# Optimization experiments

Hardware: AMD Instinct MI355X
Metric: run time of the kernel (lower is better)

The kernel has to match this reference:

```python
import jax, jax.numpy as jnp
import numpy as np

B, S, D, H = 4, 8192, 1024, 16
DH = D // H  # attention head size


def setup_inputs() -> dict:
    key = jax.random.key(0)
    ks = jax.random.split(key, 12)
    sc = 0.02
    return {
        "hidden_states": jax.random.normal(ks[0], (B, S, D), jnp.float32),
        "attention_mask": jnp.zeros((B, 1, S), jnp.float32),
        "Wq": jax.random.normal(ks[1], (D, D), jnp.float32) * sc,
        "bq": jnp.zeros((D,), jnp.float32),
        "Wqa": jax.random.normal(ks[2], (D, H), jnp.float32) * sc,
        "bqa": jnp.zeros((H,), jnp.float32),
        "Wk": jax.random.normal(ks[3], (D, D), jnp.float32) * sc,
        "bk": jnp.zeros((D,), jnp.float32),
        "Wka": jax.random.normal(ks[4], (D, H), jnp.float32) * sc,
        "bka": jnp.zeros((H,), jnp.float32),
        "Wt": jax.random.normal(ks[5], (D, D), jnp.float32) * sc,
        "bt": jnp.zeros((D,), jnp.float32),
    }


def reference(hidden_states, attention_mask, Wq, bq, Wqa, bqa, Wk, bk, Wka, bka, Wt, bt):
    b, s, _ = hidden_states.shape
    scale = 1.0 / np.sqrt(DH).astype(np.float32)

    mixed_q = hidden_states @ Wq + bq            # [B,S,D]
    mixed_k = hidden_states @ Wk + bk            # [B,S,D]

    # query attention pooling: scores [B,H,S]
    q_score = (mixed_q @ Wqa + bqa).transpose(0, 2, 1) * scale + attention_mask
    q_weight = jax.nn.softmax(q_score, axis=-1)  # [B,H,S]

    q_heads = mixed_q.reshape(b, s, H, DH)       # [B,S,H,DH]
    pooled_q = jnp.einsum("bhs,bshd->bhd", q_weight, q_heads)  # [B,H,DH]
    pooled_q = pooled_q.reshape(b, 1, D)         # global query vector per batch

    mixed_qk = mixed_k * pooled_q                # [B,S,D]

    qk_score = (mixed_qk @ Wka + bka).transpose(0, 2, 1) * scale + attention_mask
    qk_weight = jax.nn.softmax(qk_score, axis=-1)  # [B,H,S]

    k_heads = mixed_qk.reshape(b, s, H, DH)
    pooled_k = jnp.einsum("bhs,bshd->bhd", qk_weight, k_heads)  # [B,H,DH]

    weighted = (q_heads * pooled_k[:, None, :, :]).reshape(b, s, D)  # [B,S,D]
    return weighted @ Wt + bt + mixed_q
```

## Files before the change

### kernel.cpp

```cpp
#include <hip/hip_runtime.h>
#include <hip/hip_bf16.h>
#include <stdint.h>

typedef __hip_bfloat16 bf16;
typedef __attribute__((ext_vector_type(8))) short bf16x8v;
typedef __attribute__((ext_vector_type(4))) float f32x4v;

#define B_   4
#define S_   8192
#define D_   1024
#define H_   16
#define DH_  64
#define M_TOT (B_ * S_)

__device__ __forceinline__ float bf2f(bf16 x) { return __bfloat162float(x); }
__device__ __forceinline__ bf16  f2bf(float x) { return __float2bfloat16(x); }

__device__ __forceinline__ void storev(float* p, float v) { *p = v; }
__device__ __forceinline__ void storev(bf16* p, float v) { *p = f2bf(v); }

__device__ __forceinline__ void async_copy16(const void* g, void* l) {
  __builtin_amdgcn_global_load_lds(
      (const __attribute__((address_space(1))) unsigned int*)g,
      (__attribute__((address_space(3))) unsigned int*)l,
      16, 0, 0);
}

#define VMCNT(n) asm volatile("s_waitcnt vmcnt(" #n ")" ::: "memory")
__device__ __forceinline__ void barrier_() {
  asm volatile("" ::: "memory");
  __builtin_amdgcn_s_barrier();
  asm volatile("" ::: "memory");
}

__global__ __launch_bounds__(256) void prep_kernel(
    const float* __restrict__ hs, const float* __restrict__ Wq,
    const float* __restrict__ Wk, const float* __restrict__ Wqa,
    bf16* __restrict__ hs_bf, bf16* __restrict__ WqkT, bf16* __restrict__ WaqT)
{
  __shared__ float tset[32][33];
  const int blk = blockIdx.x, tid = threadIdx.x;
  if (blk < 2048) {
    const int n4 = M_TOT * D_ / 4;
    for (int i = blk * 256 + tid; i < n4; i += 2048 * 256) {
      const float4 v = ((const float4*)hs)[i];
      union { bf16 h[4]; uint64_t u; } pk;
      pk.h[0] = f2bf(v.x); pk.h[1] = f2bf(v.y);
      pk.h[2] = f2bf(v.z); pk.h[3] = f2bf(v.w);
      ((uint64_t*)hs_bf)[i] = pk.u;
    }
  } else if (blk < 4096) {
    const int t = blk - 2048;
    const int mat = t >> 10, tile = t & 1023;
    const int bx = tile & 31, by = tile >> 5;
    const float* W = mat ? Wk : Wq;
    bf16* o = WqkT + (size_t)mat * 1024 * 1024;
    const int tx = tid & 31, ty0 = tid >> 5;
#pragma unroll
    for (int r = 0; r < 4; ++r)
      tset[ty0 + 8 * r][tx] = W[(size_t)(by * 32 + ty0 + 8 * r) * D_ + bx * 32 + tx];
    __syncthreads();
#pragma unroll
    for (int r = 0; r < 4; ++r)
      o[(size_t)(bx * 32 + ty0 + 8 * r) * D_ + by * 32 + tx] = f2bf(tset[tx][ty0 + 8 * r]);
  } else {
    const int idx = (blk - 4096) * 256 + tid;
    const int d = idx & (D_ - 1), h = (idx >> 10) & 15;
    WaqT[idx] = f2bf(Wqa[d * H_ + h]);
  }
}

#define STAGE_A(nb, h, k0) do { \
  async_copy16(gA + (size_t)((h) * 64      ) * sA + (size_t)(k0) * 2, smem + (nb) + (h) * 16384 + ldsw); \
  async_copy16(gA + (size_t)((h) * 64 + 128) * sA + (size_t)(k0) * 2, smem + (nb) + (h) * 16384 + 8192 + ldsw); \
} while (0)

#define STAGE_B(nb, h, k0) do { \
  async_copy16(gB + (size_t)((h) * 32      ) * sB + (size_t)(k0) * 2, smem + (nb) + 32768 + (h) * 16384 + ldsw); \
  async_copy16(gB + (size_t)((h) * 32 + 128) * sB + (size_t)(k0) * 2, smem + (nb) + 32768 + (h) * 16384 + 8192 + ldsw); \
} while (0)

#define READ_A(mh) do { \
  _Pragma("unroll") for (int il = 0; il < 4; ++il) { \
    const uint8_t* p_ = Ab + (mh) * 16384 + (wr * 64 + il * 16 + l16) * 128; \
    a[il][0] = *(const bf16x8v*)(p_ + k0off); \
    a[il][1] = *(const bf16x8v*)(p_ + k1off); } \
} while (0)

#define READ_B(nh, BR) do { \
  _Pragma("unroll") for (int jl = 0; jl < 2; ++jl) { \
    const uint8_t* p_ = Bb + 32768 + (nh) * 16384 + (wc * 32 + jl * 16 + l16) * 128; \
    BR[jl][0] = *(const bf16x8v*)(p_ + k0off); \
    BR[jl][1] = *(const bf16x8v*)(p_ + k1off); } \
} while (0)

#define MFMA_Q(IOFF, JOFF, BR) do { \
  _Pragma("unroll") for (int il = 0; il < 4; ++il) \
  _Pragma("unroll") for (int jl = 0; jl < 2; ++jl) \
  _Pragma("unroll") for (int kk = 0; kk < 2; ++kk) \
    acc[(IOFF) + il][(JOFF) + jl] = __builtin_amdgcn_mfma_f32_16x16x32_bf16( \
        a[il][kk], BR[jl][kk], acc[(IOFF) + il][(JOFF) + jl], 0, 0, 0); \
} while (0)

template <typename OutT>
__global__ __launch_bounds__(512, 2) void gemm256_kernel(
    const bf16* __restrict__ A, int lda, const bf16* __restrict__ BT,
    const float* __restrict__ bias0, const float* __restrict__ bias1,
    const bf16* addC, int ldadd,
    OutT* __restrict__ C, int ldc, int M, int Ncols, int K, int perBatchB)
{
  extern __shared__ __align__(16) uint8_t smem[];

  const int ntile = Ncols >> 8;
  const int mtiles = M >> 8;
  const int xcd = blockIdx.x & 7;
  const int local = blockIdx.x >> 3;
  const int tn = local % ntile;
  const int tm = xcd * (mtiles >> 3) + local / ntile;
  const int m0 = tm << 8, n0 = tn << 8;
  const bf16* Bt = BT + (perBatchB ? (size_t)(m0 >> 13) * (size_t)Ncols * (size_t)K : 0);

  const int tid = threadIdx.x, w = tid >> 6, lane = tid & 63;
  const int quad = lane >> 4, l16 = lane & 15;
  const int wr = w >> 2, wc = w & 3;
  const int lr = lane >> 3, ls = lane & 7;

  const size_t sA = (size_t)lda * 2, sB = (size_t)K * 2;
  const int srcslot = (ls ^ lr) << 4;
  const uint8_t* gA = (const uint8_t*)A  + (size_t)(m0 + 8 * w + lr) * sA + srcslot;
  const uint8_t* gB = (const uint8_t*)Bt + (size_t)(n0 + 64 * wr + 8 * wc + lr) * sB + srcslot;
  const int ldsw = w << 10;

  const int e7 = l16 & 7;
  const int k0off = (quad ^ e7) << 4;
  const int k1off = ((quad + 4) ^ e7) << 4;

  f32x4v acc[8][4] = {};
  bf16x8v a[4][2], b0[2][2], b1[2][2];

  const int NT = K >> 6;

  STAGE_A(0, 0, 0);
  STAGE_B(0, 0, 0);
  STAGE_B(0, 1, 0);
  STAGE_A(0, 1, 0);
  VMCNT(4);
  barrier_();

  for (int t = 0; t < NT; ++t) {
    const int buf = (t & 1) << 16;
    const int nbuf = buf ^ 65536;
    const int kst = (t + 1 < NT ? t + 1 : t) << 6;
    const uint8_t* Ab = smem + buf;
    const uint8_t* Bb = smem + buf;

    READ_A(0);
    READ_B(0, b0);
    STAGE_A(nbuf, 0, kst);
    barrier_();
    __builtin_amdgcn_s_setprio(1);
    MFMA_Q(0, 0, b0);
    __builtin_amdgcn_s_setprio(0);
    VMCNT(4);
    barrier_();

    READ_B(1, b1);
    STAGE_B(nbuf, 0, kst);
    barrier_();
    __builtin_amdgcn_s_setprio(1);
    MFMA_Q(0, 2, b1);
    __builtin_amdgcn_s_setprio(0);
    VMCNT(4);
    barrier_();

    READ_A(1);
    STAGE_B(nbuf, 1, kst);
    barrier_();
    __builtin_amdgcn_s_setprio(1);
    MFMA_Q(4, 2, b1);
    __builtin_amdgcn_s_setprio(0);
    barrier_();

    STAGE_A(nbuf, 1, kst);
    barrier_();
    __builtin_amdgcn_s_setprio(1);
    MFMA_Q(4, 0, b0);
    __builtin_amdgcn_s_setprio(0);
    VMCNT(4);
    barrier_();
  }
  VMCNT(0);

#pragma unroll
  for (int ai = 0; ai < 8; ++ai) {
    const int row = m0 + wr * 128 + ai * 16 + quad * 4;
#pragma unroll
    for (int jb = 0; jb < 4; ++jb) {
      const int col = n0 + wc * 64 + jb * 16 + l16;
      const float bb = (col < 1024) ? (bias0 ? bias0[col] : 0.f)
                                    : (bias1 ? bias1[col - 1024] : 0.f);
      f32x4v v = acc[ai][jb];
#pragma unroll
      for (int r = 0; r < 4; ++r) {
        float o = v[r] + bb;
        if (addC) o += bf2f(addC[(size_t)(row + r) * ldadd + col]);
        storev(&C[(size_t)(row + r) * ldc + col], o);
      }
    }
  }
}

__global__ __launch_bounds__(256) void score_kernel(
    const bf16* __restrict__ X, int ldx, const bf16* __restrict__ WaT,
    const float* __restrict__ mask, float* __restrict__ scores,
    float scale, int perBatchW)
{
  const int tid = threadIdx.x, wave = tid >> 6, lane = tid & 63;
  const int quad = lane >> 4, l16 = lane & 15;
  const int row0 = blockIdx.x * 64 + wave * 16;
  const int b = row0 / S_;
  const bf16* W = WaT + (perBatchW ? (size_t)b * H_ * D_ : 0);
  const bf16* arow = X + (size_t)(row0 + l16) * ldx;
  const bf16* brow = W + (size_t)l16 * D_;
  f32x4v acc = {};
  for (int k0 = 0; k0 < D_; k0 += 32) {
    bf16x8v av = *(const bf16x8v*)(arow + k0 + quad * 8);
    bf16x8v bv = *(const bf16x8v*)(brow + k0 + quad * 8);
    acc = __builtin_amdgcn_mfma_f32_16x16x32_bf16(av, bv, acc, 0, 0, 0);
  }
  const int srel = (row0 % S_) + quad * 4;
  const float* mp = mask + (size_t)b * S_ + srel;
  float* orow = scores + ((size_t)b * H_ + l16) * S_ + srel;
#pragma unroll
  for (int r = 0; r < 4; r++) orow[r] = expf(acc[r] * scale + mp[r]);
}

__global__ __launch_bounds__(256) void pool_kernel(
    const float* __restrict__ esc, const bf16* __restrict__ X, int ldx,
    float* __restrict__ pooled, float* __restrict__ sumw)
{
  const int bh = blockIdx.x, chunk = blockIdx.y;
  const int b = bh >> 4, h = bh & 15;
  const int dh = threadIdx.x & 63, sr = threadIdx.x >> 6;
  const float* erow = esc + (size_t)bh * S_;
  float acc = 0.f, accw = 0.f;
  const int s0 = chunk * 256;
  for (int s = s0 + sr; s < s0 + 256; s += 4) {
    const float e = erow[s];
    acc += e * bf2f(X[((size_t)b * S_ + s) * ldx + h * DH_ + dh]);
    if (dh == 0) accw += e;
  }
  __shared__ float red[256];
  __shared__ float rw[4];
  red[threadIdx.x] = acc;
  if (dh == 0) rw[sr] = accw;
  __syncthreads();
  if (sr == 0)
    atomicAdd(&pooled[b * D_ + h * DH_ + dh],
              red[dh] + red[64 + dh] + red[128 + dh] + red[192 + dh]);
  if (threadIdx.x == 0)
    atomicAdd(&sumw[bh], rw[0] + rw[1] + rw[2] + rw[3]);
}

__global__ __launch_bounds__(256) void prep_wa_kernel(
    const float* __restrict__ Wa, const float* __restrict__ pq,
    const float* __restrict__ sw, bf16* __restrict__ out)
{
  const int idx = blockIdx.x * 256 + threadIdx.x;
  if (idx >= B_ * H_ * D_) return;
  const int d = idx & (D_ - 1);
  const int h = (idx >> 10) & 15;
  const int b = idx >> 14;
  const float inv = __frcp_rn(sw[b * H_ + (d >> 6)]);
  const float v = Wa[d * H_ + h] * pq[b * D_ + d] * inv;
  out[idx] = f2bf(v);
}

__global__ __launch_bounds__(1024) void transpose_scale_kernel(
    const float* __restrict__ W, const float* __restrict__ pq,
    const float* __restrict__ swq, const float* __restrict__ pk,
    const float* __restrict__ swk, bf16* __restrict__ out)
{
  __shared__ float t[32][33];
  const int tx = threadIdx.x, ty = threadIdx.y;
  const int bx = blockIdx.x, by = blockIdx.y, b = blockIdx.z;
  t[ty][tx] = W[(size_t)(by * 32 + ty) * D_ + bx * 32 + tx];
  __syncthreads();
  const int n = bx * 32 + ty, k = by * 32 + tx;
  const float invq = __frcp_rn(swq[b * H_ + (k >> 6)]);
  const float invk = __frcp_rn(swk[b * H_ + (k >> 6)]);
  const float s = (pq[b * D_ + k] * invq) * (pk[b * D_ + k] * invk);
  out[(size_t)b * D_ * D_ + (size_t)n * D_ + k] = f2bf(t[tx][ty] * s);
}

namespace {
struct LdsAttrInit {
  LdsAttrInit() {
    (void)hipFuncSetAttribute(reinterpret_cast<const void*>(&gemm256_kernel<bf16>),
                              hipFuncAttributeMaxDynamicSharedMemorySize, 131072);
    (void)hipFuncSetAttribute(reinterpret_cast<const void*>(&gemm256_kernel<float>),
                              hipFuncAttributeMaxDynamicSharedMemorySize, 131072);
  }
};
LdsAttrInit ldsAttrInit_;
}

extern "C" void kernel_launch(void* const* d_in, const int* in_sizes, int n_in,
                              void* d_out, int out_size, void* d_ws, size_t ws_size,
                              hipStream_t stream)
{
  const float* hs   = (const float*)d_in[0];
  const float* mask = (const float*)d_in[1];
  const float* Wq   = (const float*)d_in[2];
  const float* bq   = (const float*)d_in[3];
  const float* Wqa  = (const float*)d_in[4];
  const float* Wk   = (const float*)d_in[6];
  const float* bk   = (const float*)d_in[7];
  const float* Wka  = (const float*)d_in[8];
  const float* Wt   = (const float*)d_in[10];
  const float* bt   = (const float*)d_in[11];
  float* out = (float*)d_out;

  uint8_t* w = (uint8_t*)d_ws;
  bf16*  hs_bf     = (bf16*)(w + 0);
  bf16*  mixed_qk  = (bf16*)(w + 67108864);
  bf16*  WqkT      = (bf16*)(w + 201326592);
  bf16*  WtTs      = (bf16*)(w + 205520896);
  bf16*  WaqT      = (bf16*)(w + 213909504);
  bf16*  WakTs     = (bf16*)(w + 213942272);
  float* scores_q  = (float*)(w + 214073344);
  float* scores_qk = (float*)(w + 216170496);
  float* pq_raw    = (float*)(w + 218267648);
  float* pk_raw    = (float*)(w + 218284032);
  float* sumw_q    = (float*)(w + 218300416);
  float* sumw_k    = (float*)(w + 218300672);

  const bf16* mixed_q = mixed_qk;
  const bf16* mixed_k = mixed_qk + 1024;
  const int LDQK = 2048;

  const float scale = 0.125f;
  dim3 tblk(32, 32);

  hipMemsetAsync(pq_raw, 0, 2 * 16384 + 512, stream);

  prep_kernel<<<4160, 256, 0, stream>>>(hs, Wq, Wk, Wqa, hs_bf, WqkT, WaqT);

  gemm256_kernel<bf16><<<1024, 512, 131072, stream>>>(
      hs_bf, 1024, WqkT, bq, bk, nullptr, 0, mixed_qk, LDQK, M_TOT, 2048, D_, 0);

  score_kernel<<<512, 256, 0, stream>>>(mixed_q, LDQK, WaqT, mask, scores_q, scale, 0);
  pool_kernel<<<dim3(64, 32), 256, 0, stream>>>(scores_q, mixed_q, LDQK, pq_raw, sumw_q);

  prep_wa_kernel<<<256, 256, 0, stream>>>(Wka, pq_raw, sumw_q, WakTs);
  score_kernel<<<512, 256, 0, stream>>>(mixed_k, LDQK, WakTs, mask, scores_qk, scale, 1);
  pool_kernel<<<dim3(64, 32), 256, 0, stream>>>(scores_qk, mixed_k, LDQK, pk_raw, sumw_k);

  transpose_scale_kernel<<<dim3(32, 32, 4), tblk, 0, stream>>>(
      Wt, pq_raw, sumw_q, pk_raw, sumw_k, WtTs);

  gemm256_kernel<float><<<512, 512, 131072, stream>>>(
      mixed_q, LDQK, WtTs, bt, nullptr, mixed_q, LDQK, out, D_, M_TOT, D_, D_, 1);
}
```

Measured before the change: 608.5 us.

## Fuse attention score and pooling kernels to avoid re-reading activations

Merges the score computation and the weighted pooling into one kernel. Each block computes exp-scores for its 64 rows in LDS and immediately accumulates the weighted sum over the same rows, which are likely still cache-hot. This removes the intermediate score buffers and a second full pass over mixed_q/mixed_k. The cost is more atomicAdds, one per column per 64-row block instead of one per column per 256-row chunk, plus a block barrier.

```diff
diff --git a/kernel.cpp b/kernel.cpp
--- a/kernel.cpp
+++ b/kernel.cpp
@@ -15,6 +15,10 @@
 
 __device__ __forceinline__ float bf2f(bf16 x) { return __bfloat162float(x); }
 __device__ __forceinline__ bf16  f2bf(float x) { return __float2bfloat16(x); }
+__device__ __forceinline__ float u16tof(unsigned short u) {
+  const unsigned int x = ((unsigned int)u) << 16;
+  return __builtin_bit_cast(float, x);
+}
 
 __device__ __forceinline__ void storev(float* p, float v) { *p = v; }
 __device__ __forceinline__ void storev(bf16* p, float v) { *p = f2bf(v); }
@@ -210,17 +214,19 @@
   }
 }
 
-__global__ __launch_bounds__(256) void score_kernel(
+__global__ __launch_bounds__(256) void score_pool_kernel(
     const bf16* __restrict__ X, int ldx, const bf16* __restrict__ WaT,
-    const float* __restrict__ mask, float* __restrict__ scores,
-    float scale, int perBatchW)
-{
+    const float* __restrict__ mask, float* __restrict__ pooled,
+    float* __restrict__ sumw, float scale, int perBatchW)
+{
+  __shared__ float e_lds[16][65];
   const int tid = threadIdx.x, wave = tid >> 6, lane = tid & 63;
   const int quad = lane >> 4, l16 = lane & 15;
-  const int row0 = blockIdx.x * 64 + wave * 16;
+  const int row0 = blockIdx.x * 64;
   const int b = row0 / S_;
   const bf16* W = WaT + (perBatchW ? (size_t)b * H_ * D_ : 0);
-  const bf16* arow = X + (size_t)(row0 + l16) * ldx;
+
+  const bf16* arow = X + (size_t)(row0 + wave * 16 + l16) * ldx;
   const bf16* brow = W + (size_t)l16 * D_;
   f32x4v acc = {};
   for (int k0 = 0; k0 < D_; k0 += 32) {
@@ -228,38 +234,37 @@
     bf16x8v bv = *(const bf16x8v*)(brow + k0 + quad * 8);
     acc = __builtin_amdgcn_mfma_f32_16x16x32_bf16(av, bv, acc, 0, 0, 0);
   }
-  const int srel = (row0 % S_) + quad * 4;
-  const float* mp = mask + (size_t)b * S_ + srel;
-  float* orow = scores + ((size_t)b * H_ + l16) * S_ + srel;
-#pragma unroll
-  for (int r = 0; r < 4; r++) orow[r] = expf(acc[r] * scale + mp[r]);
-}
-
-__global__ __launch_bounds__(256) void pool_kernel(
-    const float* __restrict__ esc, const bf16* __restrict__ X, int ldx,
-    float* __restrict__ pooled, float* __restrict__ sumw)
-{
-  const int bh = blockIdx.x, chunk = blockIdx.y;
-  const int b = bh >> 4, h = bh & 15;
-  const int dh = threadIdx.x & 63, sr = threadIdx.x >> 6;
-  const float* erow = esc + (size_t)bh * S_;
-  float acc = 0.f, accw = 0.f;
-  const int s0 = chunk * 256;
-  for (int s = s0 + sr; s < s0 + 256; s += 4) {
-    const float e = erow[s];
-    acc += e * bf2f(X[((size_t)b * S_ + s) * ldx + h * DH_ + dh]);
-    if (dh == 0) accw += e;
-  }
-  __shared__ float red[256];
-  __shared__ float rw[4];
-  red[threadIdx.x] = acc;
-  if (dh == 0) rw[sr] = accw;
+  const int srel = wave * 16 + quad * 4;
+  const float* mp = mask + row0 + srel;
+#pragma unroll
+  for (int r = 0; r < 4; ++r)
+    e_lds[l16][srel + r] = expf(acc[r] * scale + mp[r]);
   __syncthreads();
-  if (sr == 0)
-    atomicAdd(&pooled[b * D_ + h * DH_ + dh],
-              red[dh] + red[64 + dh] + red[128 + dh] + red[192 + dh]);
-  if (threadIdx.x == 0)
-    atomicAdd(&sumw[bh], rw[0] + rw[1] + rw[2] + rw[3]);
+
+  const int c0 = tid * 4;
+  const int h = c0 >> 6;
+  float p0 = 0.f, p1 = 0.f, p2 = 0.f, p3 = 0.f;
+  const bf16* xb = X + (size_t)row0 * ldx + c0;
+#pragma unroll 4
+  for (int s = 0; s < 64; ++s) {
+    const float e = e_lds[h][s];
+    const ushort4 xv = *(const ushort4*)(xb + (size_t)s * ldx);
+    p0 += e * u16tof(xv.x);
+    p1 += e * u16tof(xv.y);
+    p2 += e * u16tof(xv.z);
+    p3 += e * u16tof(xv.w);
+  }
+  float* pd = pooled + (size_t)b * D_ + c0;
+  atomicAdd(pd + 0, p0);
+  atomicAdd(pd + 1, p1);
+  atomicAdd(pd + 2, p2);
+  atomicAdd(pd + 3, p3);
+  if (tid < 16) {
+    float sum = 0.f;
+#pragma unroll 8
+    for (int s = 0; s < 64; ++s) sum += e_lds[tid][s];
+    atomicAdd(&sumw[b * H_ + tid], sum);
+  }
 }
 
 __global__ __launch_bounds__(256) void prep_wa_kernel(
@@ -328,8 +333,6 @@
   bf16*  WtTs      = (bf16*)(w + 205520896);
   bf16*  WaqT      = (bf16*)(w + 213909504);
   bf16*  WakTs     = (bf16*)(w + 213942272);
-  float* scores_q  = (float*)(w + 214073344);
-  float* scores_qk = (float*)(w + 216170496);
   float* pq_raw    = (float*)(w + 218267648);
   float* pk_raw    = (float*)(w + 218284032);
   float* sumw_q    = (float*)(w + 218300416);
@@ -349,12 +352,12 @@
   gemm256_kernel<bf16><<<1024, 512, 131072, stream>>>(
       hs_bf, 1024, WqkT, bq, bk, nullptr, 0, mixed_qk, LDQK, M_TOT, 2048, D_, 0);
 
-  score_kernel<<<512, 256, 0, stream>>>(mixed_q, LDQK, WaqT, mask, scores_q, scale, 0);
-  pool_kernel<<<dim3(64, 32), 256, 0, stream>>>(scores_q, mixed_q, LDQK, pq_raw, sumw_q);
+  score_pool_kernel<<<512, 256, 0, stream>>>(
+      mixed_q, LDQK, WaqT, mask, pq_raw, sumw_q, scale, 0);
 
   prep_wa_kernel<<<256, 256, 0, stream>>>(Wka, pq_raw, sumw_q, WakTs);
-  score_kernel<<<512, 256, 0, stream>>>(mixed_k, LDQK, WakTs, mask, scores_qk, scale, 1);
-  pool_kernel<<<dim3(64, 32), 256, 0, stream>>>(scores_qk, mixed_k, LDQK, pk_raw, sumw_k);
+  score_pool_kernel<<<512, 256, 0, stream>>>(
+      mixed_k, LDQK, WakTs, mask, pk_raw, sumw_k, scale, 1);
 
   transpose_scale_kernel<<<dim3(32, 32, 4), tblk, 0, stream>>>(
       Wt, pq_raw, sumw_q, pk_raw, sumw_k, WtTs);
```

Result: no change. 603.1 us (-0.9%).
